# Optimization experiments

Hardware: AMD Instinct MI355X
Metric: run time of the kernel (lower is better)

## Reference

```python
import jax, jax.numpy as jnp
import numpy as np

N, DEG, D_IN, D_HID = 50000, 16, 963, 256


def setup_inputs() -> dict:
    key = jax.random.key(0)
    ks = jax.random.split(key, 8)
    s = 0.02
    neighbours = jax.random.randint(ks[0], (N, DEG), 0, N)
    shape_features = jax.random.normal(ks[1], (N, D_IN), dtype=jnp.float32)
    # layer 0: D_IN -> D_HID; layers 1..13 (stacked): D_HID -> D_HID; extra: D_HID -> 3
    W_self0 = jax.random.normal(ks[2], (D_IN, D_HID), dtype=jnp.float32) * s
    W_neigh0 = jax.random.normal(ks[3], (D_IN, D_HID), dtype=jnp.float32) * s
    b0 = jnp.zeros((D_HID,), jnp.float32)
    W_self = jax.random.normal(ks[4], (13, D_HID, D_HID), dtype=jnp.float32) * s
    W_neigh = jax.random.normal(ks[5], (13, D_HID, D_HID), dtype=jnp.float32) * s
    b = jnp.zeros((13, D_HID), jnp.float32)
    W_extra = jax.random.normal(ks[6], (D_HID, 3), dtype=jnp.float32) * s
    b_extra = jnp.zeros((3,), jnp.float32)
    return {
        "neighbours": neighbours,
        "shape_features": shape_features,
        "W_self0": W_self0, "W_neigh0": W_neigh0, "b0": b0,
        "W_self": W_self, "W_neigh": W_neigh, "b": b,
        "W_extra": W_extra, "b_extra": b_extra,
    }


def _gcn(x, neighbours, Ws, Wn, bias):
    # gather neighbour features [N, DEG, D] and sum-aggregate, plus self transform
    agg = jnp.take(x, neighbours, axis=0).sum(axis=1)
    return x @ Ws + agg @ Wn + bias


def reference(neighbours, shape_features, W_self0, W_neigh0, b0, W_self, W_neigh, b, W_extra, b_extra):
    x = jax.nn.relu(_gcn(shape_features, neighbours, W_self0, W_neigh0, b0))
    for i in range(6):  # 6 residual blocks of 2 GCN layers each
        temp = x
        x = jax.nn.relu(_gcn(x, neighbours, W_self[2 * i], W_neigh[2 * i], b[2 * i]))
        x = jax.nn.relu(_gcn(x, neighbours, W_self[2 * i + 1], W_neigh[2 * i + 1], b[2 * i + 1]))
        x = (temp + x) / 2
    x = jax.nn.relu(_gcn(x, neighbours, W_self[12], W_neigh[12], b[12]))
    coordinates = x @ W_extra + b_extra  # extra layer called without neighbours -> linear
    return (x, coordinates)
```

## Files before the change

kernel.cpp:

```cpp
#include <hip/hip_runtime.h>
#include <hip/hip_bf16.h>
#include <hip/hip_fp16.h>
#include <stdint.h>

#define NNODES 50000
#define NPAD   50048
#define DEG    16
#define DIN    963
#define K0PAD  992
#define DHID   256
#define SCALE  (1.0f / 1024.0f)
#define ISCALE 1024.0f

typedef __attribute__((ext_vector_type(4))) float    f32x4;
typedef __attribute__((ext_vector_type(8))) _Float16 f16x8;
typedef __attribute__((ext_vector_type(4))) _Float16 f16x4;

typedef const __attribute__((address_space(1))) void GV;
typedef __attribute__((address_space(3))) void LV;

__device__ __forceinline__ void gl2lds16(const void* g, void* l) {
    __builtin_amdgcn_global_load_lds((GV*)g, (LV*)l, 16, 0, 0);
}

__global__ __launch_bounds__(256) void gemm_mfma(
    const _Float16* __restrict__ A, int K,
    const _Float16* __restrict__ Wp,
    _Float16* __restrict__ ys, _Float16* __restrict__ yn)
{
    __shared__ _Float16 lds[2][2][4096];

    const int tid  = threadIdx.x;
    const int w    = tid >> 6;
    const int lane = tid & 63;
    const int bm   = blockIdx.x * 128;
    const int nb   = blockIdx.y * 128;

    const int KT = K >> 5;

    auto stage = [&](int s, int kt) {
        const int k0 = kt << 5;
#pragma unroll
        for (int i = 0; i < 2; ++i) {
            const int j   = w + (i << 2);
            const int c   = (j << 6) + lane;
            const int row = c & 127;
            const int k8  = (c >> 7) << 3;
            gl2lds16(A  + (size_t)(bm + row) * K + k0 + k8, &lds[s][0][(size_t)j << 9]);
            gl2lds16(Wp + (size_t)(nb + row) * K + k0 + k8, &lds[s][1][(size_t)j << 9]);
        }
    };

    const int wm = (w >> 1) << 6;
    const int wn = (w & 1) << 6;
    const int lr = lane & 15;
    const int kh = lane >> 4;

    f32x4 acc[4][4] = {};

    stage(0, 0);
    __syncthreads();
    int cur = 0;
    for (int kt = 0; kt < KT; ++kt) {
        if (kt + 1 < KT) stage(cur ^ 1, kt + 1);
        f16x8 a[4], b[4];
#pragma unroll
        for (int mi = 0; mi < 4; ++mi)
            a[mi] = *(const f16x8*)&lds[cur][0][((kh << 7) + wm + (mi << 4) + lr) << 3];
#pragma unroll
        for (int ni = 0; ni < 4; ++ni)
            b[ni] = *(const f16x8*)&lds[cur][1][((kh << 7) + wn + (ni << 4) + lr) << 3];
#pragma unroll
        for (int mi = 0; mi < 4; ++mi)
#pragma unroll
            for (int ni = 0; ni < 4; ++ni)
                acc[mi][ni] = __builtin_amdgcn_mfma_f32_16x16x32_f16(a[mi], b[ni], acc[mi][ni], 0, 0, 0);
        __syncthreads();
        cur ^= 1;
    }

    _Float16* C = (blockIdx.y < 2) ? ys : yn;
    const int cb = (nb & 255) + wn;
#pragma unroll
    for (int mi = 0; mi < 4; ++mi) {
        const size_t rbase = (size_t)(bm + wm + (mi << 4) + (kh << 2)) << 8;
#pragma unroll
        for (int ni = 0; ni < 4; ++ni) {
            const int col = cb + (ni << 4) + lr;
#pragma unroll
            for (int r = 0; r < 4; ++r)
                C[rbase + ((size_t)r << 8) + col] = (_Float16)acc[mi][ni][r];
        }
    }
}

__global__ __launch_bounds__(256) void combine(
    const _Float16* __restrict__ ys, const _Float16* __restrict__ yn,
    const int* __restrict__ nbr, const float* __restrict__ bias,
    const _Float16* __restrict__ res,
    _Float16* __restrict__ outh, float* __restrict__ outf)
{
    const int n = blockIdx.x;
    const int c = threadIdx.x;
    __shared__ int nb[DEG];
    if (c < DEG) nb[c] = nbr[n * DEG + c];
    __syncthreads();
    float s = (float)ys[((size_t)n << 8) + c] + bias[c] * SCALE;
#pragma unroll
    for (int j = 0; j < DEG; ++j)
        s += (float)yn[((size_t)nb[j] << 8) + c];
    s = fmaxf(s, 0.f);
    if (res) s = ((float)res[((size_t)n << 8) + c] + s) * 0.5f;
    if (outh) outh[((size_t)n << 8) + c] = (_Float16)s;
    else      outf[((size_t)n << 8) + c] = s * ISCALE;
}

__global__ __launch_bounds__(64) void coords_kernel(
    const float* __restrict__ x, const float* __restrict__ We,
    const float* __restrict__ be, float* __restrict__ out3, int N)
{
    const int n = blockIdx.x;
    const int l = threadIdx.x;
    const float4 xv = *(const float4*)(x + (size_t)n * 256 + l * 4);
    float p0 = 0.f, p1 = 0.f, p2 = 0.f;
    const float xs[4] = {xv.x, xv.y, xv.z, xv.w};
#pragma unroll
    for (int i = 0; i < 4; ++i) {
        const int cidx = l * 4 + i;
        p0 += xs[i] * We[cidx * 3 + 0];
        p1 += xs[i] * We[cidx * 3 + 1];
        p2 += xs[i] * We[cidx * 3 + 2];
    }
#pragma unroll
    for (int off = 32; off > 0; off >>= 1) {
        p0 += __shfl_down(p0, off);
        p1 += __shfl_down(p1, off);
        p2 += __shfl_down(p2, off);
    }
    if (l == 0) {
        out3[(size_t)n * 3 + 0] = p0 + be[0];
        out3[(size_t)n * 3 + 1] = p1 + be[1];
        out3[(size_t)n * 3 + 2] = p2 + be[2];
    }
}

__global__ __launch_bounds__(256) void conv_sf(const float* __restrict__ sf,
                                               _Float16* __restrict__ sfb)
{
    const int idx = blockIdx.x * 256 + threadIdx.x;
    const int row = idx / (K0PAD / 4);
    const int k4  = (idx % (K0PAD / 4)) * 4;
    f16x4 o;
#pragma unroll
    for (int i = 0; i < 4; ++i) {
        const int k = k4 + i;
        float v = (row < NNODES && k < DIN) ? sf[(size_t)row * DIN + k] * SCALE : 0.f;
        o[i] = (_Float16)v;
    }
    *(f16x4*)(sfb + (size_t)row * K0PAD + k4) = o;
}

__global__ __launch_bounds__(256) void pack_w0(const float* __restrict__ Ws0,
                                               const float* __restrict__ Wn0,
                                               _Float16* __restrict__ Wp0)
{
    const int idx = blockIdx.x * 256 + threadIdx.x;
    const int k  = idx >> 9;
    const int nn = idx & 511;
    float v = 0.f;
    if (k < DIN) v = (nn < 256) ? Ws0[(size_t)k * 256 + nn]
                                : Wn0[(size_t)k * 256 + (nn - 256)];
    Wp0[(size_t)nn * K0PAD + k] = (_Float16)v;
}

__global__ __launch_bounds__(256) void pack_w(const float* __restrict__ Ws,
                                              const float* __restrict__ Wn,
                                              _Float16* __restrict__ Wpk)
{
    const int idx = blockIdx.x * 256 + threadIdx.x;
    const int l   = idx >> 17;
    const int rem = idx & 131071;
    const int k   = rem >> 9;
    const int nn  = rem & 511;
    const float v = (nn < 256) ? Ws[(size_t)l * 65536 + k * 256 + nn]
                               : Wn[(size_t)l * 65536 + k * 256 + (nn - 256)];
    Wpk[(size_t)l * 131072 + (size_t)nn * 256 + k] = (_Float16)v;
}

extern "C" void kernel_launch(void* const* d_in, const int* in_sizes, int n_in,
                              void* d_out, int out_size, void* d_ws, size_t ws_size,
                              hipStream_t stream)
{
    const int*   nbr = (const int*)d_in[0];
    const float* sf  = (const float*)d_in[1];
    const float* Ws0 = (const float*)d_in[2];
    const float* Wn0 = (const float*)d_in[3];
    const float* b0  = (const float*)d_in[4];
    const float* Ws  = (const float*)d_in[5];
    const float* Wn  = (const float*)d_in[6];
    const float* bb  = (const float*)d_in[7];
    const float* We  = (const float*)d_in[8];
    const float* be  = (const float*)d_in[9];
    float* out = (float*)d_out;

    uint8_t* w = (uint8_t*)d_ws;
    _Float16* sfb = (_Float16*)w;
    _Float16* P   = (_Float16*)w;
    _Float16* Q   = P + (size_t)NPAD * 256;
    _Float16* Wpk = Q + (size_t)NPAD * 256;
    _Float16* Wp0 = (_Float16*)(w + (size_t)NPAD * K0PAD * 2);
    _Float16* ysb = Wp0 + (size_t)512 * K0PAD;
    _Float16* ynb = ysb + (size_t)NPAD * 256;

    conv_sf<<<NPAD * (K0PAD / 4) / 256, 256, 0, stream>>>(sf, sfb);
    pack_w0<<<512 * K0PAD / 256, 256, 0, stream>>>(Ws0, Wn0, Wp0);

    const dim3 gg(NPAD / 128, 4);

    gemm_mfma<<<gg, 256, 0, stream>>>(sfb, K0PAD, Wp0, ysb, ynb);
    pack_w<<<13 * 512 * 256 / 256, 256, 0, stream>>>(Ws, Wn, Wpk);
    combine<<<NNODES, 256, 0, stream>>>(ysb, ynb, nbr, b0, nullptr, P, nullptr);

    for (int t = 0; t < 6; ++t) {
        const int lA = 2 * t, lB = lA + 1;
        gemm_mfma<<<gg, 256, 0, stream>>>(P, 256, Wpk + (size_t)lA * 131072, ysb, ynb);
        combine<<<NNODES, 256, 0, stream>>>(ysb, ynb, nbr, bb + lA * 256, nullptr, Q, nullptr);
        gemm_mfma<<<gg, 256, 0, stream>>>(Q, 256, Wpk + (size_t)lB * 131072, ysb, ynb);
        combine<<<NNODES, 256, 0, stream>>>(ysb, ynb, nbr, bb + lB * 256, P, P, nullptr);
    }

    gemm_mfma<<<gg, 256, 0, stream>>>(P, 256, Wpk + (size_t)12 * 131072, ysb, ynb);
    combine<<<NNODES, 256, 0, stream>>>(ysb, ynb, nbr, bb + 12 * 256, nullptr, nullptr, out);

    coords_kernel<<<NNODES, 64, 0, stream>>>(out, We, be, out + (size_t)NNODES * 256, NNODES);
}
```

Baseline: 1.633 ms.

## Widen GEMM tiles to 128x256 with XCD-aware remap and vectorize combine/pack kernels

The GEMM now uses 512-thread blocks computing 128x256 output tiles, so each A tile is loaded once per output half rather than twice, and blocks are remapped so neighbouring tiles land on the same XCD. The combine kernel processes four nodes per block, with each lane handling four channels through vector loads, which cuts block count and per-element gather overhead. The conversion and weight-packing kernels now write 8-wide f16 vectors. Risks are higher LDS and register pressure in the GEMM, which may lower occupancy, and the remap formula must cover every tile exactly once.

```diff
diff --git a/kernel.cpp b/kernel.cpp
--- a/kernel.cpp
+++ b/kernel.cpp
@@ -23,36 +23,46 @@
     __builtin_amdgcn_global_load_lds((GV*)g, (LV*)l, 16, 0, 0);
 }
 
-__global__ __launch_bounds__(256) void gemm_mfma(
+__global__ __launch_bounds__(512) void gemm_mfma(
     const _Float16* __restrict__ A, int K,
     const _Float16* __restrict__ Wp,
     _Float16* __restrict__ ys, _Float16* __restrict__ yn)
 {
-    __shared__ _Float16 lds[2][2][4096];
+    __shared__ _Float16 ldsA[2][4096];
+    __shared__ _Float16 ldsB[2][8192];
 
     const int tid  = threadIdx.x;
     const int w    = tid >> 6;
     const int lane = tid & 63;
-    const int bm   = blockIdx.x * 128;
-    const int nb   = blockIdx.y * 128;
+
+    const int nwg = gridDim.x;
+    const int bid = blockIdx.x;
+    const int q = nwg >> 3, r = nwg & 7, xc = bid & 7;
+    const int wgid = (xc < r ? xc * (q + 1) : r * (q + 1) + (xc - r) * q) + (bid >> 3);
+    const int bm = (wgid >> 1) << 7;
+    const int by = wgid & 1;
+    const int nb = by << 8;
 
     const int KT = K >> 5;
 
     auto stage = [&](int s, int kt) {
         const int k0 = kt << 5;
+        {
+            const int c = (w << 6) + lane;
+            gl2lds16(A + (size_t)(bm + (c & 127)) * K + k0 + ((c >> 7) << 3),
+                     &ldsA[s][(size_t)w << 9]);
+        }
 #pragma unroll
         for (int i = 0; i < 2; ++i) {
-            const int j   = w + (i << 2);
-            const int c   = (j << 6) + lane;
-            const int row = c & 127;
-            const int k8  = (c >> 7) << 3;
-            gl2lds16(A  + (size_t)(bm + row) * K + k0 + k8, &lds[s][0][(size_t)j << 9]);
-            gl2lds16(Wp + (size_t)(nb + row) * K + k0 + k8, &lds[s][1][(size_t)j << 9]);
+            const int j = w + (i << 3);
+            const int c = (j << 6) + lane;
+            gl2lds16(Wp + (size_t)(nb + (c & 255)) * K + k0 + ((c >> 8) << 3),
+                     &ldsB[s][(size_t)j << 9]);
         }
     };
 
-    const int wm = (w >> 1) << 6;
-    const int wn = (w & 1) << 6;
+    const int wm = (w >> 2) << 6;
+    const int wn = (w & 3) << 6;
     const int lr = lane & 15;
     const int kh = lane >> 4;
 
@@ -66,10 +76,10 @@
         f16x8 a[4], b[4];
 #pragma unroll
         for (int mi = 0; mi < 4; ++mi)
-            a[mi] = *(const f16x8*)&lds[cur][0][((kh << 7) + wm + (mi << 4) + lr) << 3];
+            a[mi] = *(const f16x8*)&ldsA[cur][((kh << 7) + wm + (mi << 4) + lr) << 3];
 #pragma unroll
         for (int ni = 0; ni < 4; ++ni)
-            b[ni] = *(const f16x8*)&lds[cur][1][((kh << 7) + wn + (ni << 4) + lr) << 3];
+            b[ni] = *(const f16x8*)&ldsB[cur][((kh << 8) + wn + (ni << 4) + lr) << 3];
 #pragma unroll
         for (int mi = 0; mi < 4; ++mi)
 #pragma unroll
@@ -79,14 +89,13 @@
         cur ^= 1;
     }
 
-    _Float16* C = (blockIdx.y < 2) ? ys : yn;
-    const int cb = (nb & 255) + wn;
+    _Float16* C = (by == 0) ? ys : yn;
 #pragma unroll
     for (int mi = 0; mi < 4; ++mi) {
         const size_t rbase = (size_t)(bm + wm + (mi << 4) + (kh << 2)) << 8;
 #pragma unroll
         for (int ni = 0; ni < 4; ++ni) {
-            const int col = cb + (ni << 4) + lr;
+            const int col = wn + (ni << 4) + lr;
 #pragma unroll
             for (int r = 0; r < 4; ++r)
                 C[rbase + ((size_t)r << 8) + col] = (_Float16)acc[mi][ni][r];
@@ -100,19 +109,41 @@
     const _Float16* __restrict__ res,
     _Float16* __restrict__ outh, float* __restrict__ outf)
 {
-    const int n = blockIdx.x;
-    const int c = threadIdx.x;
-    __shared__ int nb[DEG];
-    if (c < DEG) nb[c] = nbr[n * DEG + c];
-    __syncthreads();
-    float s = (float)ys[((size_t)n << 8) + c] + bias[c] * SCALE;
-#pragma unroll
-    for (int j = 0; j < DEG; ++j)
-        s += (float)yn[((size_t)nb[j] << 8) + c];
-    s = fmaxf(s, 0.f);
-    if (res) s = ((float)res[((size_t)n << 8) + c] + s) * 0.5f;
-    if (outh) outh[((size_t)n << 8) + c] = (_Float16)s;
-    else      outf[((size_t)n << 8) + c] = s * ISCALE;
+    const int w    = threadIdx.x >> 6;
+    const int lane = threadIdx.x & 63;
+    const int n    = (blockIdx.x << 2) + w;
+    const int c4   = lane << 2;
+    const size_t base = ((size_t)n << 8) + c4;
+
+    const f16x4 ysv = *(const f16x4*)(ys + base);
+    const float4 bv = *(const float4*)(bias + c4);
+    float s0 = (float)ysv[0] + bv.x * SCALE;
+    float s1 = (float)ysv[1] + bv.y * SCALE;
+    float s2 = (float)ysv[2] + bv.z * SCALE;
+    float s3 = (float)ysv[3] + bv.w * SCALE;
+
+    const int* nr = nbr + n * DEG;
+#pragma unroll
+    for (int j = 0; j < DEG; ++j) {
+        const f16x4 v = *(const f16x4*)(yn + (((size_t)nr[j]) << 8) + c4);
+        s0 += (float)v[0]; s1 += (float)v[1]; s2 += (float)v[2]; s3 += (float)v[3];
+    }
+    s0 = fmaxf(s0, 0.f); s1 = fmaxf(s1, 0.f); s2 = fmaxf(s2, 0.f); s3 = fmaxf(s3, 0.f);
+    if (res) {
+        const f16x4 rv = *(const f16x4*)(res + base);
+        s0 = ((float)rv[0] + s0) * 0.5f;
+        s1 = ((float)rv[1] + s1) * 0.5f;
+        s2 = ((float)rv[2] + s2) * 0.5f;
+        s3 = ((float)rv[3] + s3) * 0.5f;
+    }
+    if (outh) {
+        f16x4 o;
+        o[0] = (_Float16)s0; o[1] = (_Float16)s1; o[2] = (_Float16)s2; o[3] = (_Float16)s3;
+        *(f16x4*)(outh + base) = o;
+    } else {
+        float4 o = make_float4(s0 * ISCALE, s1 * ISCALE, s2 * ISCALE, s3 * ISCALE);
+        *(float4*)(outf + base) = o;
+    }
 }
 
 __global__ __launch_bounds__(64) void coords_kernel(
@@ -148,16 +179,17 @@
                                                _Float16* __restrict__ sfb)
 {
     const int idx = blockIdx.x * 256 + threadIdx.x;
-    const int row = idx / (K0PAD / 4);
-    const int k4  = (idx % (K0PAD / 4)) * 4;
-    f16x4 o;
-#pragma unroll
-    for (int i = 0; i < 4; ++i) {
-        const int k = k4 + i;
-        float v = (row < NNODES && k < DIN) ? sf[(size_t)row * DIN + k] * SCALE : 0.f;
-        o[i] = (_Float16)v;
-    }
-    *(f16x4*)(sfb + (size_t)row * K0PAD + k4) = o;
+    const int row = idx / 124;
+    const int k8  = (idx % 124) << 3;
+    f16x8 o = {};
+    if (row < NNODES) {
+#pragma unroll
+        for (int i = 0; i < 8; ++i) {
+            const int k = k8 + i;
+            o[i] = (k < DIN) ? (_Float16)(sf[(size_t)row * DIN + k] * SCALE) : (_Float16)0.f;
+        }
+    }
+    *(f16x8*)(sfb + (size_t)row * K0PAD + k8) = o;
 }
 
 __global__ __launch_bounds__(256) void pack_w0(const float* __restrict__ Ws0,
@@ -165,12 +197,17 @@
                                                _Float16* __restrict__ Wp0)
 {
     const int idx = blockIdx.x * 256 + threadIdx.x;
-    const int k  = idx >> 9;
-    const int nn = idx & 511;
-    float v = 0.f;
-    if (k < DIN) v = (nn < 256) ? Ws0[(size_t)k * 256 + nn]
-                                : Wn0[(size_t)k * 256 + (nn - 256)];
-    Wp0[(size_t)nn * K0PAD + k] = (_Float16)v;
+    const int nn  = idx & 511;
+    const int k8  = idx >> 9;
+    const float* W = (nn < 256) ? Ws0 : Wn0;
+    const int n0 = nn & 255;
+    f16x8 o;
+#pragma unroll
+    for (int i = 0; i < 8; ++i) {
+        const int k = (k8 << 3) + i;
+        o[i] = (k < DIN) ? (_Float16)W[(size_t)k * 256 + n0] : (_Float16)0.f;
+    }
+    *(f16x8*)(Wp0 + (size_t)nn * K0PAD + (k8 << 3)) = o;
 }
 
 __global__ __launch_bounds__(256) void pack_w(const float* __restrict__ Ws,
@@ -178,13 +215,16 @@
                                               _Float16* __restrict__ Wpk)
 {
     const int idx = blockIdx.x * 256 + threadIdx.x;
-    const int l   = idx >> 17;
-    const int rem = idx & 131071;
-    const int k   = rem >> 9;
-    const int nn  = rem & 511;
-    const float v = (nn < 256) ? Ws[(size_t)l * 65536 + k * 256 + nn]
-                               : Wn[(size_t)l * 65536 + k * 256 + (nn - 256)];
-    Wpk[(size_t)l * 131072 + (size_t)nn * 256 + k] = (_Float16)v;
+    const int nn  = idx & 511;
+    const int k8  = (idx >> 9) & 31;
+    const int l   = idx >> 14;
+    const float* W = (nn < 256) ? Ws : Wn;
+    const int n0 = nn & 255;
+    f16x8 o;
+#pragma unroll
+    for (int i = 0; i < 8; ++i)
+        o[i] = (_Float16)W[(size_t)l * 65536 + ((k8 << 3) + i) * 256 + n0];
+    *(f16x8*)(Wpk + (size_t)l * 131072 + (size_t)nn * 256 + (k8 << 3)) = o;
 }
 
 extern "C" void kernel_launch(void* const* d_in, const int* in_sizes, int n_in,
@@ -212,25 +252,25 @@
     _Float16* ysb = Wp0 + (size_t)512 * K0PAD;
     _Float16* ynb = ysb + (size_t)NPAD * 256;
 
-    conv_sf<<<NPAD * (K0PAD / 4) / 256, 256, 0, stream>>>(sf, sfb);
-    pack_w0<<<512 * K0PAD / 256, 256, 0, stream>>>(Ws0, Wn0, Wp0);
-
-    const dim3 gg(NPAD / 128, 4);
-
-    gemm_mfma<<<gg, 256, 0, stream>>>(sfb, K0PAD, Wp0, ysb, ynb);
-    pack_w<<<13 * 512 * 256 / 256, 256, 0, stream>>>(Ws, Wn, Wpk);
-    combine<<<NNODES, 256, 0, stream>>>(ysb, ynb, nbr, b0, nullptr, P, nullptr);
+    conv_sf<<<NPAD * 124 / 256, 256, 0, stream>>>(sf, sfb);
+    pack_w0<<<512 * 124 / 256, 256, 0, stream>>>(Ws0, Wn0, Wp0);
+
+    const int gemmGrid = (NPAD / 128) * 2;
+
+    gemm_mfma<<<gemmGrid, 512, 0, stream>>>(sfb, K0PAD, Wp0, ysb, ynb);
+    pack_w<<<13 * 512 * 32 / 256, 256, 0, stream>>>(Ws, Wn, Wpk);
+    combine<<<NNODES / 4, 256, 0, stream>>>(ysb, ynb, nbr, b0, nullptr, P, nullptr);
 
     for (int t = 0; t < 6; ++t) {
         const int lA = 2 * t, lB = lA + 1;
-        gemm_mfma<<<gg, 256, 0, stream>>>(P, 256, Wpk + (size_t)lA * 131072, ysb, ynb);
-        combine<<<NNODES, 256, 0, stream>>>(ysb, ynb, nbr, bb + lA * 256, nullptr, Q, nullptr);
-        gemm_mfma<<<gg, 256, 0, stream>>>(Q, 256, Wpk + (size_t)lB * 131072, ysb, ynb);
-        combine<<<NNODES, 256, 0, stream>>>(ysb, ynb, nbr, bb + lB * 256, P, P, nullptr);
-    }
-
-    gemm_mfma<<<gg, 256, 0, stream>>>(P, 256, Wpk + (size_t)12 * 131072, ysb, ynb);
-    combine<<<NNODES, 256, 0, stream>>>(ysb, ynb, nbr, bb + 12 * 256, nullptr, nullptr, out);
+        gemm_mfma<<<gemmGrid, 512, 0, stream>>>(P, 256, Wpk + (size_t)lA * 131072, ysb, ynb);
+        combine<<<NNODES / 4, 256, 0, stream>>>(ysb, ynb, nbr, bb + lA * 256, nullptr, Q, nullptr);
+        gemm_mfma<<<gemmGrid, 512, 0, stream>>>(Q, 256, Wpk + (size_t)lB * 131072, ysb, ynb);
+        combine<<<NNODES / 4, 256, 0, stream>>>(ysb, ynb, nbr, bb + lB * 256, P, P, nullptr);
+    }
+
+    gemm_mfma<<<gemmGrid, 512, 0, stream>>>(P, 256, Wpk + (size_t)12 * 131072, ysb, ynb);
+    combine<<<NNODES / 4, 256, 0, stream>>>(ysb, ynb, nbr, bb + 12 * 256, nullptr, nullptr, out);
 
     coords_kernel<<<NNODES, 64, 0, stream>>>(out, We, be, out + (size_t)NNODES * 256, NNODES);
 }
```

Result: faster. 1.599 ms (-2.1%).
